# Performance work log

Hardware: AMD Instinct MI355X
Metric: run time of the kernel (lower is better)

The kernel has to match this reference:

```python
import jax, jax.numpy as jnp
import numpy as np


def _hadamard(n):
    # Sylvester construction; n must be a power of 2 (matches scipy.linalg.hadamard)
    H = np.array([[1.0]], dtype=np.float32)
    while H.shape[0] < n:
        H = np.block([[H, H], [H, -H]])
    return jnp.asarray(H)


def setup_inputs() -> dict:
    key = jax.random.key(0)
    k1, k2 = jax.random.split(key)
    shape = (524288, 3, 8, 8)  # [num_blocks, channels, 8, 8] SATD blocks
    return {
        "original": jax.random.normal(k1, shape, dtype=jnp.float32),
        "pred": jax.random.normal(k2, shape, dtype=jnp.float32),
    }


def reference(original, pred):
    n = original.shape[-1]  # last dim sizes the Hadamard matrix, as in the torch code
    H = _hadamard(n)  # [n, n]
    diff = original - pred  # [B, C, n, n]
    # torch.matmul(H, block): contract H columns with block rows (dim -2)
    t = jnp.einsum('ij,bcjw->bciw', H, diff)
    return jnp.sum(jnp.abs(t))
```

## Files before the change

### kernel.cpp

```cpp
#include <hip/hip_runtime.h>


__device__ __forceinline__ float4 f4add(float4 a, float4 b) {
    return make_float4(a.x + b.x, a.y + b.y, a.z + b.z, a.w + b.w);
}
__device__ __forceinline__ float4 f4sub(float4 a, float4 b) {
    return make_float4(a.x - b.x, a.y - b.y, a.z - b.z, a.w - b.w);
}
__device__ __forceinline__ float f4abssum(float4 a) {
    return fabsf(a.x) + fabsf(a.y) + fabsf(a.z) + fabsf(a.w);
}

__global__ __launch_bounds__(256) void satd_loss_kernel(
        const float* __restrict__ orig, const float* __restrict__ pred,
        float* __restrict__ out, int nwork) {
    const int tid = blockIdx.x * blockDim.x + threadIdx.x;
    const int gstride = gridDim.x * blockDim.x;

    float acc = 0.0f;

    for (int i = tid; i < nwork; i += gstride) {
        const int base = (i >> 1) * 64 + (i & 1) * 4;

        float4 d0, d1, d2, d3, d4, d5, d6, d7;
        {
            const float4* o = reinterpret_cast<const float4*>(orig + base);
            const float4* p = reinterpret_cast<const float4*>(pred + base);
            d0 = f4sub(o[0],  p[0]);
            d1 = f4sub(o[2],  p[2]);
            d2 = f4sub(o[4],  p[4]);
            d3 = f4sub(o[6],  p[6]);
            d4 = f4sub(o[8],  p[8]);
            d5 = f4sub(o[10], p[10]);
            d6 = f4sub(o[12], p[12]);
            d7 = f4sub(o[14], p[14]);
        }

        float4 a0 = f4add(d0, d1), a1 = f4sub(d0, d1);
        float4 a2 = f4add(d2, d3), a3 = f4sub(d2, d3);
        float4 a4 = f4add(d4, d5), a5 = f4sub(d4, d5);
        float4 a6 = f4add(d6, d7), a7 = f4sub(d6, d7);

        float4 b0 = f4add(a0, a2), b2 = f4sub(a0, a2);
        float4 b1 = f4add(a1, a3), b3 = f4sub(a1, a3);
        float4 b4 = f4add(a4, a6), b6 = f4sub(a4, a6);
        float4 b5 = f4add(a5, a7), b7 = f4sub(a5, a7);

        float4 c0 = f4add(b0, b4), c4 = f4sub(b0, b4);
        float4 c1 = f4add(b1, b5), c5 = f4sub(b1, b5);
        float4 c2 = f4add(b2, b6), c6 = f4sub(b2, b6);
        float4 c3 = f4add(b3, b7), c7 = f4sub(b3, b7);

        acc += f4abssum(c0) + f4abssum(c1) + f4abssum(c2) + f4abssum(c3)
             + f4abssum(c4) + f4abssum(c5) + f4abssum(c6) + f4abssum(c7);
    }

    #pragma unroll
    for (int off = 32; off > 0; off >>= 1)
        acc += __shfl_down(acc, off, 64);

    __shared__ float wsum[4];
    const int lane = threadIdx.x & 63;
    const int wid  = threadIdx.x >> 6;
    if (lane == 0) wsum[wid] = acc;
    __syncthreads();

    if (threadIdx.x == 0) {
        float s = wsum[0] + wsum[1] + wsum[2] + wsum[3];
        atomicAdd(out, s);
    }
}

extern "C" void kernel_launch(void* const* d_in, const int* in_sizes, int n_in,
                              void* d_out, int out_size, void* d_ws, size_t ws_size,
                              hipStream_t stream) {
    const float* orig = (const float*)d_in[0];
    const float* pred = (const float*)d_in[1];
    float* out = (float*)d_out;

    const int nelem = in_sizes[0];
    const int nwork = nelem / 32;

    hipMemsetAsync(out, 0, sizeof(float) * (size_t)out_size, stream);

    const int block = 256;
    int grid = 4096;
    const int needed = (nwork + block - 1) / block;
    if (needed < grid) grid = needed;

    satd_loss_kernel<<<grid, block, 0, stream>>>(orig, pred, out, nwork);
}
```

Baseline: 146.5 us.

## Use contiguous coalesced float4 loads with cross-lane shuffle Hadamard butterfly

Each thread now loads consecutive float4 chunks, so a wavefront reads fully contiguous memory. The 8-point Hadamard across rows is done with xor-shuffles between lanes (masks 2, 4, 8), where before each thread loaded eight strided rows. Loads are nontemporal and four chunks are batched per loop iteration to raise memory-level parallelism. The cost is extra shuffle instructions. Correctness depends on row alignment to lane groups, which holds only if gstride is a multiple of 16.

```diff
diff --git a/kernel.cpp b/kernel.cpp
--- a/kernel.cpp
+++ b/kernel.cpp
@@ -1,58 +1,48 @@
 #include <hip/hip_runtime.h>
 
 
-__device__ __forceinline__ float4 f4add(float4 a, float4 b) {
-    return make_float4(a.x + b.x, a.y + b.y, a.z + b.z, a.w + b.w);
-}
-__device__ __forceinline__ float4 f4sub(float4 a, float4 b) {
-    return make_float4(a.x - b.x, a.y - b.y, a.z - b.z, a.w - b.w);
-}
-__device__ __forceinline__ float f4abssum(float4 a) {
-    return fabsf(a.x) + fabsf(a.y) + fabsf(a.z) + fabsf(a.w);
-}
+typedef float fvec4 __attribute__((ext_vector_type(4)));
 
 __global__ __launch_bounds__(256) void satd_loss_kernel(
-        const float* __restrict__ orig, const float* __restrict__ pred,
-        float* __restrict__ out, int nwork) {
+        const fvec4* __restrict__ orig, const fvec4* __restrict__ pred,
+        float* __restrict__ out, int n4) {
     const int tid = blockIdx.x * blockDim.x + threadIdx.x;
     const int gstride = gridDim.x * blockDim.x;
+    const int lane = threadIdx.x & 63;
 
     float acc = 0.0f;
 
-    for (int i = tid; i < nwork; i += gstride) {
-        const int base = (i >> 1) * 64 + (i & 1) * 4;
-
-        float4 d0, d1, d2, d3, d4, d5, d6, d7;
-        {
-            const float4* o = reinterpret_cast<const float4*>(orig + base);
-            const float4* p = reinterpret_cast<const float4*>(pred + base);
-            d0 = f4sub(o[0],  p[0]);
-            d1 = f4sub(o[2],  p[2]);
-            d2 = f4sub(o[4],  p[4]);
-            d3 = f4sub(o[6],  p[6]);
-            d4 = f4sub(o[8],  p[8]);
-            d5 = f4sub(o[10], p[10]);
-            d6 = f4sub(o[12], p[12]);
-            d7 = f4sub(o[14], p[14]);
+    for (int base = tid; base < n4; base += gstride * 4) {
+        fvec4 v[4];
+        #pragma unroll
+        for (int k = 0; k < 4; ++k) {
+            const int idx = base + k * gstride;
+            if (idx < n4) {
+                fvec4 a = __builtin_nontemporal_load(&orig[idx]);
+                fvec4 b = __builtin_nontemporal_load(&pred[idx]);
+                v[k] = a - b;
+            } else {
+                v[k] = (fvec4)(0.f);
+            }
         }
 
-        float4 a0 = f4add(d0, d1), a1 = f4sub(d0, d1);
-        float4 a2 = f4add(d2, d3), a3 = f4sub(d2, d3);
-        float4 a4 = f4add(d4, d5), a5 = f4sub(d4, d5);
-        float4 a6 = f4add(d6, d7), a7 = f4sub(d6, d7);
-
-        float4 b0 = f4add(a0, a2), b2 = f4sub(a0, a2);
-        float4 b1 = f4add(a1, a3), b3 = f4sub(a1, a3);
-        float4 b4 = f4add(a4, a6), b6 = f4sub(a4, a6);
-        float4 b5 = f4add(a5, a7), b7 = f4sub(a5, a7);
-
-        float4 c0 = f4add(b0, b4), c4 = f4sub(b0, b4);
-        float4 c1 = f4add(b1, b5), c5 = f4sub(b1, b5);
-        float4 c2 = f4add(b2, b6), c6 = f4sub(b2, b6);
-        float4 c3 = f4add(b3, b7), c7 = f4sub(b3, b7);
-
-        acc += f4abssum(c0) + f4abssum(c1) + f4abssum(c2) + f4abssum(c3)
-             + f4abssum(c4) + f4abssum(c5) + f4abssum(c6) + f4abssum(c7);
+        #pragma unroll
+        for (int k = 0; k < 4; ++k) {
+            fvec4 t = v[k];
+            #pragma unroll
+            for (int m = 2; m <= 8; m <<= 1) {
+                const bool hi = (lane & m) != 0;
+                fvec4 p;
+                p.x = __shfl_xor(t.x, m, 64);
+                p.y = __shfl_xor(t.y, m, 64);
+                p.z = __shfl_xor(t.z, m, 64);
+                p.w = __shfl_xor(t.w, m, 64);
+                fvec4 add = t + p;
+                fvec4 sub = p - t;
+                t = hi ? sub : add;
+            }
+            acc += fabsf(t.x) + fabsf(t.y) + fabsf(t.z) + fabsf(t.w);
+        }
     }
 
     #pragma unroll
@@ -60,8 +50,7 @@
         acc += __shfl_down(acc, off, 64);
 
     __shared__ float wsum[4];
-    const int lane = threadIdx.x & 63;
-    const int wid  = threadIdx.x >> 6;
+    const int wid = threadIdx.x >> 6;
     if (lane == 0) wsum[wid] = acc;
     __syncthreads();
 
@@ -74,19 +63,17 @@
 extern "C" void kernel_launch(void* const* d_in, const int* in_sizes, int n_in,
                               void* d_out, int out_size, void* d_ws, size_t ws_size,
                               hipStream_t stream) {
-    const float* orig = (const float*)d_in[0];
-    const float* pred = (const float*)d_in[1];
+    const fvec4* orig = (const fvec4*)d_in[0];
+    const fvec4* pred = (const fvec4*)d_in[1];
     float* out = (float*)d_out;
 
     const int nelem = in_sizes[0];
-    const int nwork = nelem / 32;
+    const int n4 = nelem / 4;
 
-    hipMemsetAsync(out, 0, sizeof(float) * (size_t)out_size, stream);
+    (void)hipMemsetAsync(out, 0, sizeof(float) * (size_t)out_size, stream);
 
     const int block = 256;
-    int grid = 4096;
-    const int needed = (nwork + block - 1) / block;
-    if (needed < grid) grid = needed;
+    const int grid = 4096;
 
-    satd_loss_kernel<<<grid, block, 0, stream>>>(orig, pred, out, nwork);
+    satd_loss_kernel<<<grid, block, 0, stream>>>(orig, pred, out, n4);
 }
```

New measurement: 148.7 us. Within noise of the previous version (+1.4%).
